# Performance work log

Hardware: AMD Instinct MI355X
Metric: run time of the kernel (lower is better)

The kernel has to match this reference:

```python
import jax, jax.numpy as jnp
import numpy as np

N_NODES = 50000
N_EDGES = 800000
D_IN = 128
D_HID = 128
N_CLASSES = 16
N_GRAPHS = 256


def _gcn_norm(edge_index, num_nodes):
    # PyG GCNConv default: add self-loops, symmetric normalization.
    loops = jnp.arange(num_nodes, dtype=edge_index.dtype)
    src = jnp.concatenate([edge_index[0], loops])
    dst = jnp.concatenate([edge_index[1], loops])
    deg = jax.ops.segment_sum(jnp.ones_like(src, dtype=jnp.float32), dst,
                              num_segments=num_nodes)
    dinv = jnp.where(deg > 0, jax.lax.rsqrt(deg), 0.0)
    norm = dinv[src] * dinv[dst]  # [E + N]
    return src, dst, norm


def _gcn_conv(x, src, dst, norm, W, b, num_nodes):
    h = x @ W                                  # [N, d_out] dense GEMM
    msg = h[src] * norm[:, None]               # gather + scale [E+N, d_out]
    agg = jax.ops.segment_sum(msg, dst, num_segments=num_nodes)
    return agg + b


def setup_inputs() -> dict:
    key = jax.random.key(0)
    ks = jax.random.split(key, 10)
    x = jax.random.normal(ks[0], (N_NODES, D_IN), dtype=jnp.float32)
    edge_index = jax.random.randint(ks[1], (2, N_EDGES), 0, N_NODES, dtype=jnp.int64)
    batch = jnp.sort(jax.random.randint(ks[2], (N_NODES,), 0, N_GRAPHS, dtype=jnp.int64))
    s1 = 1.0 / np.sqrt(D_IN)
    s2 = 1.0 / np.sqrt(D_HID)
    W1 = jax.random.uniform(ks[3], (D_IN, D_HID), jnp.float32, -s1, s1)
    b1 = jnp.zeros((D_HID,), jnp.float32)
    W2 = jax.random.uniform(ks[4], (D_HID, D_HID), jnp.float32, -s2, s2)
    b2 = jnp.zeros((D_HID,), jnp.float32)
    Wc = jax.random.uniform(ks[5], (D_HID, N_CLASSES), jnp.float32, -s2, s2)
    bc = jnp.zeros((N_CLASSES,), jnp.float32)
    return {"x": x, "edge_index": edge_index, "batch": batch,
            "W1": W1, "b1": b1, "W2": W2, "b2": b2, "Wc": Wc, "bc": bc}


def reference(x, edge_index, batch, W1, b1, W2, b2, Wc, bc):
    src, dst, norm = _gcn_norm(edge_index, N_NODES)
    h = _gcn_conv(x, src, dst, norm, W1, b1, N_NODES)
    h = jax.nn.relu(h)  # dropout is identity in eval mode
    h = _gcn_conv(h, src, dst, norm, W2, b2, N_NODES)
    # global mean pool over graph ids
    sums = jax.ops.segment_sum(h, batch, num_segments=N_GRAPHS)
    cnts = jax.ops.segment_sum(jnp.ones((N_NODES,), jnp.float32), batch,
                               num_segments=N_GRAPHS)
    pooled = sums / jnp.maximum(cnts, 1.0)[:, None]  # [G, D_HID]
    return pooled @ Wc + bc  # [G, N_CLASSES]
```

## Files before the change

### kernel.cpp

```cpp
#include <hip/hip_runtime.h>

#define N_NODES 50000
#define N_EDGES 800000
#define D 128
#define N_GRAPHS 256
#define N_CLASSES 16
#define NB_DINV ((N_NODES + 255) / 256)
#define BKT 64

typedef unsigned short ushort_t;
typedef unsigned int uint_t;
typedef unsigned char uchar_t;
typedef __attribute__((ext_vector_type(8))) short bf16x8;
typedef __attribute__((ext_vector_type(4))) float f32x4;
typedef __attribute__((ext_vector_type(4))) int i32x4;

__device__ __forceinline__ float bf2f(uint_t u) {
  return __uint_as_float(u << 16);
}
__device__ __forceinline__ uint_t f2bf(float f) {
  uint_t x = __float_as_uint(f);
  return (x + 0x7fffu + ((x >> 16) & 1u)) >> 16;
}
__device__ __forceinline__ void add8(float* acc, uint4 v) {
  acc[0] += bf2f(v.x & 0xffffu);
  acc[1] += bf2f(v.x >> 16);
  acc[2] += bf2f(v.y & 0xffffu);
  acc[3] += bf2f(v.y >> 16);
  acc[4] += bf2f(v.z & 0xffffu);
  acc[5] += bf2f(v.z >> 16);
  acc[6] += bf2f(v.w & 0xffffu);
  acc[7] += bf2f(v.w >> 16);
}

__global__ void k_pre(const int* __restrict__ ei, int* __restrict__ deg,
                      int* __restrict__ csr) {
  int e = blockIdx.x * blockDim.x + threadIdx.x;
  if (e >= N_EDGES) return;
  int s = ei[e];
  int d = ei[N_EDGES + e];
  int r = atomicAdd(&deg[d], 1);
  if (r < BKT) __builtin_nontemporal_store(s, csr + d * BKT + r);
}

__global__ __launch_bounds__(256) void k_prep(const int* __restrict__ deg,
                                              float* __restrict__ dinv,
                                              const float* __restrict__ W1,
                                              const float* __restrict__ W2,
                                              uint4* __restrict__ W1f,
                                              uint4* __restrict__ W2f,
                                              const int* __restrict__ batch,
                                              float* __restrict__ rcnts) {
  int t = threadIdx.x;
  int b = blockIdx.x;
  if (b < NB_DINV) {
    int i = b * 256 + t;
    if (i < N_NODES) dinv[i] = rsqrtf((float)(deg[i] + 1));
    return;
  }
  if (b < NB_DINV + 16) {
    int slot = (b - NB_DINV) * 256 + t;
    const float* W = (slot < 2048) ? W1 : W2;
    uint4* Wf = (slot < 2048) ? W1f : W2f;
    int sl = slot & 2047;
    int lane = sl & 63;
    int s = (sl >> 6) & 3;
    int n = sl >> 8;
    int col = n * 16 + (lane & 15);
    int k0 = s * 32 + (lane >> 4) * 8;
    uint4 o;
    o.x = f2bf(W[(size_t)(k0 + 0) * D + col]) | (f2bf(W[(size_t)(k0 + 1) * D + col]) << 16);
    o.y = f2bf(W[(size_t)(k0 + 2) * D + col]) | (f2bf(W[(size_t)(k0 + 3) * D + col]) << 16);
    o.z = f2bf(W[(size_t)(k0 + 4) * D + col]) | (f2bf(W[(size_t)(k0 + 5) * D + col]) << 16);
    o.w = f2bf(W[(size_t)(k0 + 6) * D + col]) | (f2bf(W[(size_t)(k0 + 7) * D + col]) << 16);
    Wf[sl] = o;
    return;
  }
  __shared__ int bound[257];
  {
    int g = t;
    int lo = 0, hi = N_NODES;
    while (lo < hi) {
      int m = (lo + hi) >> 1;
      if (batch[m] < g) lo = m + 1; else hi = m;
    }
    bound[g] = lo;
    if (t == 255) bound[256] = N_NODES;
  }
  __syncthreads();
  int cnt = bound[t + 1] - bound[t];
  rcnts[t] = 1.0f / (float)max(cnt, 1);
}

template <typename TIN>
__global__ __launch_bounds__(256) void k_gemm_mfma(const TIN* __restrict__ A,
                                                   const uint4* __restrict__ Wf,
                                                   const float* __restrict__ dinv,
                                                   ushort_t* __restrict__ Out) {
  __shared__ uint4 As[1024];
  int t = threadIdx.x;
  int row0 = blockIdx.x * 64;
  if constexpr (sizeof(TIN) == 4) {
    uint2* As2 = (uint2*)As;
#pragma unroll
    for (int i = 0; i < 8; ++i) {
      int F = t + 256 * i;
      int r = F >> 5, f = F & 31;
      int grow = row0 + r;
      uint2 u = make_uint2(0, 0);
      if (grow < N_NODES) {
        float4 v = *(const float4*)(A + (size_t)grow * D + f * 4);
        u.x = f2bf(v.x) | (f2bf(v.y) << 16);
        u.y = f2bf(v.z) | (f2bf(v.w) << 16);
      }
      int g = f >> 1;
      As2[(r * 16 + (g ^ (r & 7))) * 2 + (f & 1)] = u;
    }
  } else {
#pragma unroll
    for (int i = 0; i < 4; ++i) {
      int G = t + 256 * i;
      int r = G >> 4, g = G & 15;
      int grow = row0 + r;
      uint4 u = make_uint4(0, 0, 0, 0);
      if (grow < N_NODES) u = *(const uint4*)(A + (size_t)grow * D + g * 8);
      As[r * 16 + (g ^ (r & 7))] = u;
    }
  }
  __syncthreads();
  int wv = t >> 6, lane = t & 63;
  int row16 = lane & 15, chunk = lane >> 4;
  int rl = wv * 16 + row16;
  bf16x8 afrag[4];
#pragma unroll
  for (int s = 0; s < 4; ++s) {
    int g = s * 4 + chunk;
    afrag[s] = *(const bf16x8*)&As[rl * 16 + (g ^ (rl & 7))];
  }
  f32x4 acc[8];
#pragma unroll
  for (int n = 0; n < 8; ++n) acc[n] = (f32x4){0.f, 0.f, 0.f, 0.f};
  const bf16x8* Wb = (const bf16x8*)Wf;
#pragma unroll
  for (int n = 0; n < 8; ++n) {
#pragma unroll
    for (int s = 0; s < 4; ++s) {
      bf16x8 b = Wb[(n * 4 + s) * 64 + lane];
      acc[n] = __builtin_amdgcn_mfma_f32_16x16x32_bf16(afrag[s], b, acc[n], 0, 0, 0);
    }
  }
  int row0w = row0 + wv * 16;
  int crow0 = row0w + chunk * 4;
  float dv[4];
#pragma unroll
  for (int j = 0; j < 4; ++j)
    dv[j] = (crow0 + j < N_NODES) ? dinv[crow0 + j] : 0.f;
#pragma unroll
  for (int n = 0; n < 8; ++n) {
#pragma unroll
    for (int j = 0; j < 4; ++j) {
      int r = crow0 + j;
      if (r < N_NODES)
        Out[(size_t)r * D + n * 16 + row16] = (ushort_t)f2bf(acc[n][j] * dv[j]);
    }
  }
}

__device__ __forceinline__ void agg_core(const ushort_t* __restrict__ h,
                                         const int* __restrict__ csr,
                                         int beg, int end, int grp, int d0,
                                         float* acc) {
  for (int wb = beg; wb < end; wb += 16) {
    int i0 = wb + grp * 4;
    i32x4 s4 = __builtin_nontemporal_load((const i32x4*)(csr + i0));
    bool b0 = i0 < end, b1 = i0 + 1 < end, b2 = i0 + 2 < end, b3 = i0 + 3 < end;
    uint4 v0, v1, v2, v3;
    if (b0) v0 = *(const uint4*)(h + (size_t)s4.x * D + d0);
    if (b1) v1 = *(const uint4*)(h + (size_t)s4.y * D + d0);
    if (b2) v2 = *(const uint4*)(h + (size_t)s4.z * D + d0);
    if (b3) v3 = *(const uint4*)(h + (size_t)s4.w * D + d0);
    if (b0) add8(acc, v0);
    if (b1) add8(acc, v1);
    if (b2) add8(acc, v2);
    if (b3) add8(acc, v3);
  }
}

__global__ __launch_bounds__(256) void k_agg_relu(const ushort_t* __restrict__ h,
                                                  const int* __restrict__ csr,
                                                  const int* __restrict__ deg,
                                                  const float* __restrict__ dinv,
                                                  const float* __restrict__ bias,
                                                  ushort_t* __restrict__ obf) {
  int t = threadIdx.x;
  int wv = t >> 6, lane = t & 63;
  int grp = lane >> 4, gl = lane & 15;
  int d0 = gl * 8;
  int node = blockIdx.x * 4 + wv;
  int beg = node * BKT, end = beg + min(deg[node], BKT);
  float acc[8] = {0.f, 0.f, 0.f, 0.f, 0.f, 0.f, 0.f, 0.f};
  agg_core(h, csr, beg, end, grp, d0, acc);
#pragma unroll
  for (int m = 16; m <= 32; m <<= 1) {
#pragma unroll
    for (int i = 0; i < 8; ++i) acc[i] += __shfl_xor(acc[i], m);
  }
  if (grp == 0) {
    uint4 v = *(const uint4*)(h + (size_t)node * D + d0);
    add8(acc, v);
    float sc = dinv[node];
    float4 blo = *(const float4*)(bias + d0);
    float4 bhi = *(const float4*)(bias + d0 + 4);
    acc[0] = fmaf(acc[0], sc, blo.x);
    acc[1] = fmaf(acc[1], sc, blo.y);
    acc[2] = fmaf(acc[2], sc, blo.z);
    acc[3] = fmaf(acc[3], sc, blo.w);
    acc[4] = fmaf(acc[4], sc, bhi.x);
    acc[5] = fmaf(acc[5], sc, bhi.y);
    acc[6] = fmaf(acc[6], sc, bhi.z);
    acc[7] = fmaf(acc[7], sc, bhi.w);
#pragma unroll
    for (int i = 0; i < 8; ++i) acc[i] = fmaxf(acc[i], 0.f);
    uint4 o;
    o.x = f2bf(acc[0]) | (f2bf(acc[1]) << 16);
    o.y = f2bf(acc[2]) | (f2bf(acc[3]) << 16);
    o.z = f2bf(acc[4]) | (f2bf(acc[5]) << 16);
    o.w = f2bf(acc[6]) | (f2bf(acc[7]) << 16);
    *(uint4*)(obf + (size_t)node * D + d0) = o;
  }
}

__global__ __launch_bounds__(1024) void k_agg_pool(const ushort_t* __restrict__ h,
                                                   const int* __restrict__ csr,
                                                   const int* __restrict__ deg,
                                                   const float* __restrict__ dinv,
                                                   const int* __restrict__ batch,
                                                   const float* __restrict__ rcnts,
                                                   float* __restrict__ sums) {
  __shared__ float pool2[16][128];
  int t = threadIdx.x;
  int wv = t >> 6, lane = t & 63;
  int grp = lane >> 4, gl = lane & 15;
  int d0 = gl * 8;
  int node0 = blockIdx.x * 16;
  int node = node0 + wv;
  int g0 = batch[node0];
  int beg = node * BKT, end = beg + min(deg[node], BKT);
  float acc[8] = {0.f, 0.f, 0.f, 0.f, 0.f, 0.f, 0.f, 0.f};
  agg_core(h, csr, beg, end, grp, d0, acc);
#pragma unroll
  for (int m = 16; m <= 32; m <<= 1) {
#pragma unroll
    for (int k = 0; k < 8; ++k) acc[k] += __shfl_xor(acc[k], m);
  }
  if (grp == 0) {
    uint4 v = *(const uint4*)(h + (size_t)node * D + d0);
    add8(acc, v);
    int g = batch[node];
    float sc = dinv[node] * rcnts[g];
    if (g == g0) {
#pragma unroll
      for (int k = 0; k < 8; ++k) pool2[wv][d0 + k] = acc[k] * sc;
    } else {
#pragma unroll
      for (int k = 0; k < 8; ++k) {
        pool2[wv][d0 + k] = 0.f;
        atomicAdd(&sums[(size_t)g * D + d0 + k], acc[k] * sc);
      }
    }
  }
  __syncthreads();
  if (t < 128) {
    float s = 0.f;
#pragma unroll
    for (int w = 0; w < 16; ++w) s += pool2[w][t];
    atomicAdd(&sums[(size_t)g0 * D + t], s);
  }
}

__global__ __launch_bounds__(128) void k_final(const float* __restrict__ sums,
                                               const float* __restrict__ b2,
                                               const float* __restrict__ Wc,
                                               const float* __restrict__ bc,
                                               float* __restrict__ out) {
  __shared__ float p[128];
  int g = blockIdx.x;
  int t = threadIdx.x;
  p[t] = sums[g * D + t] + b2[t];
  __syncthreads();
  if (t < N_CLASSES) {
    float acc = bc[t];
    for (int k = 0; k < D; ++k) acc = fmaf(p[k], Wc[k * N_CLASSES + t], acc);
    out[g * N_CLASSES + t] = acc;
  }
}

extern "C" void kernel_launch(void* const* d_in, const int* in_sizes, int n_in,
                              void* d_out, int out_size, void* d_ws, size_t ws_size,
                              hipStream_t stream) {
  const float* x = (const float*)d_in[0];
  const int* ei = (const int*)d_in[1];
  const int* batch = (const int*)d_in[2];
  const float* W1 = (const float*)d_in[3];
  const float* b1 = (const float*)d_in[4];
  const float* W2 = (const float*)d_in[5];
  const float* b2 = (const float*)d_in[6];
  const float* Wc = (const float*)d_in[7];
  const float* bc = (const float*)d_in[8];
  float* out = (float*)d_out;

  char* ws = (char*)d_ws;
  size_t off = 0;
  auto alloc = [&](size_t bytes) -> void* {
    void* p = (void*)(ws + off);
    off += (bytes + 255) & ~(size_t)255;
    return p;
  };
  int* deg = (int*)alloc((size_t)N_NODES * 4);
  float* sums = (float*)alloc((size_t)N_GRAPHS * D * 4);
  size_t zero_bytes = off;
  float* dinv = (float*)alloc((size_t)N_NODES * 4);
  float* rcnts = (float*)alloc((size_t)N_GRAPHS * 4);
  uint4* W1f = (uint4*)alloc((size_t)2048 * 16);
  uint4* W2f = (uint4*)alloc((size_t)2048 * 16);
  int* csr = (int*)alloc((size_t)N_NODES * BKT * 4);
  ushort_t* hbuf = (ushort_t*)alloc((size_t)N_NODES * D * 2);
  ushort_t* x2 = (ushort_t*)alloc((size_t)N_NODES * D * 2);

  hipMemsetAsync(ws, 0, zero_bytes, stream);

  k_pre<<<(N_EDGES + 255) / 256, 256, 0, stream>>>(ei, deg, csr);
  k_prep<<<NB_DINV + 17, 256, 0, stream>>>(deg, dinv, W1, W2, W1f, W2f, batch, rcnts);

  k_gemm_mfma<float><<<(N_NODES + 63) / 64, 256, 0, stream>>>(x, W1f, dinv, hbuf);
  k_agg_relu<<<N_NODES / 4, 256, 0, stream>>>(hbuf, csr, deg, dinv, b1, x2);
  k_gemm_mfma<ushort_t><<<(N_NODES + 63) / 64, 256, 0, stream>>>(x2, W2f, dinv, hbuf);
  k_agg_pool<<<N_NODES / 16, 1024, 0, stream>>>(hbuf, csr, deg, dinv, batch, rcnts, sums);

  k_final<<<N_GRAPHS, 128, 0, stream>>>(sums, b2, Wc, bc, out);
}
```

Measured before the change: 249.4 us.

## Merge CSR build with first GEMM and apply source degree norm during aggregation

Removes the separate dinv array and the dinv scaling in the GEMM epilogue. Aggregation now computes rsqrt(deg+1) per gathered source edge and uses an FMA in place of the add. Because the GEMM no longer needs dinv, the edge-bucketing work and the first GEMM run as disjoint block ranges of one kernel, saving a launch and letting the two overlap. The cost is an extra scattered deg load and rsqrt per edge in both aggregation kernels, plus mixing atomic-heavy blocks with GEMM blocks in one grid.

```diff
diff --git a/kernel.cpp b/kernel.cpp
--- a/kernel.cpp
+++ b/kernel.cpp
@@ -5,12 +5,12 @@
 #define D 128
 #define N_GRAPHS 256
 #define N_CLASSES 16
-#define NB_DINV ((N_NODES + 255) / 256)
 #define BKT 64
+#define NGEMM ((N_NODES + 63) / 64)
+#define NPRE ((N_EDGES + 255) / 256)
 
 typedef unsigned short ushort_t;
 typedef unsigned int uint_t;
-typedef unsigned char uchar_t;
 typedef __attribute__((ext_vector_type(8))) short bf16x8;
 typedef __attribute__((ext_vector_type(4))) float f32x4;
 typedef __attribute__((ext_vector_type(4))) int i32x4;
@@ -22,44 +22,27 @@
   uint_t x = __float_as_uint(f);
   return (x + 0x7fffu + ((x >> 16) & 1u)) >> 16;
 }
-__device__ __forceinline__ void add8(float* acc, uint4 v) {
-  acc[0] += bf2f(v.x & 0xffffu);
-  acc[1] += bf2f(v.x >> 16);
-  acc[2] += bf2f(v.y & 0xffffu);
-  acc[3] += bf2f(v.y >> 16);
-  acc[4] += bf2f(v.z & 0xffffu);
-  acc[5] += bf2f(v.z >> 16);
-  acc[6] += bf2f(v.w & 0xffffu);
-  acc[7] += bf2f(v.w >> 16);
-}
-
-__global__ void k_pre(const int* __restrict__ ei, int* __restrict__ deg,
-                      int* __restrict__ csr) {
-  int e = blockIdx.x * blockDim.x + threadIdx.x;
-  if (e >= N_EDGES) return;
-  int s = ei[e];
-  int d = ei[N_EDGES + e];
-  int r = atomicAdd(&deg[d], 1);
-  if (r < BKT) __builtin_nontemporal_store(s, csr + d * BKT + r);
-}
-
-__global__ __launch_bounds__(256) void k_prep(const int* __restrict__ deg,
-                                              float* __restrict__ dinv,
-                                              const float* __restrict__ W1,
-                                              const float* __restrict__ W2,
-                                              uint4* __restrict__ W1f,
-                                              uint4* __restrict__ W2f,
-                                              const int* __restrict__ batch,
-                                              float* __restrict__ rcnts) {
+__device__ __forceinline__ void fma8(float* acc, float w, uint4 v) {
+  acc[0] = fmaf(w, bf2f(v.x & 0xffffu), acc[0]);
+  acc[1] = fmaf(w, bf2f(v.x >> 16), acc[1]);
+  acc[2] = fmaf(w, bf2f(v.y & 0xffffu), acc[2]);
+  acc[3] = fmaf(w, bf2f(v.y >> 16), acc[3]);
+  acc[4] = fmaf(w, bf2f(v.z & 0xffffu), acc[4]);
+  acc[5] = fmaf(w, bf2f(v.z >> 16), acc[5]);
+  acc[6] = fmaf(w, bf2f(v.w & 0xffffu), acc[6]);
+  acc[7] = fmaf(w, bf2f(v.w >> 16), acc[7]);
+}
+
+__global__ __launch_bounds__(256) void k_prep0(const float* __restrict__ W1,
+                                               const float* __restrict__ W2,
+                                               uint4* __restrict__ W1f,
+                                               uint4* __restrict__ W2f,
+                                               const int* __restrict__ batch,
+                                               float* __restrict__ rcnts) {
   int t = threadIdx.x;
   int b = blockIdx.x;
-  if (b < NB_DINV) {
-    int i = b * 256 + t;
-    if (i < N_NODES) dinv[i] = rsqrtf((float)(deg[i] + 1));
-    return;
-  }
-  if (b < NB_DINV + 16) {
-    int slot = (b - NB_DINV) * 256 + t;
+  if (b < 16) {
+    int slot = b * 256 + t;
     const float* W = (slot < 2048) ? W1 : W2;
     uint4* Wf = (slot < 2048) ? W1f : W2f;
     int sl = slot & 2047;
@@ -93,13 +76,11 @@
 }
 
 template <typename TIN>
-__global__ __launch_bounds__(256) void k_gemm_mfma(const TIN* __restrict__ A,
-                                                   const uint4* __restrict__ Wf,
-                                                   const float* __restrict__ dinv,
-                                                   ushort_t* __restrict__ Out) {
-  __shared__ uint4 As[1024];
-  int t = threadIdx.x;
-  int row0 = blockIdx.x * 64;
+__device__ __forceinline__ void gemm_body(const TIN* __restrict__ A,
+                                          const uint4* __restrict__ Wf,
+                                          ushort_t* __restrict__ Out,
+                                          uint4* As, int bid, int t) {
+  int row0 = bid * 64;
   if constexpr (sizeof(TIN) == 4) {
     uint2* As2 = (uint2*)As;
 #pragma unroll
@@ -149,25 +130,50 @@
       acc[n] = __builtin_amdgcn_mfma_f32_16x16x32_bf16(afrag[s], b, acc[n], 0, 0, 0);
     }
   }
-  int row0w = row0 + wv * 16;
-  int crow0 = row0w + chunk * 4;
-  float dv[4];
-#pragma unroll
-  for (int j = 0; j < 4; ++j)
-    dv[j] = (crow0 + j < N_NODES) ? dinv[crow0 + j] : 0.f;
+  int crow0 = row0 + wv * 16 + chunk * 4;
 #pragma unroll
   for (int n = 0; n < 8; ++n) {
 #pragma unroll
     for (int j = 0; j < 4; ++j) {
       int r = crow0 + j;
       if (r < N_NODES)
-        Out[(size_t)r * D + n * 16 + row16] = (ushort_t)f2bf(acc[n][j] * dv[j]);
-    }
-  }
+        Out[(size_t)r * D + n * 16 + row16] = (ushort_t)f2bf(acc[n][j]);
+    }
+  }
+}
+
+__global__ __launch_bounds__(256) void k_mega(const float* __restrict__ x,
+                                              const int* __restrict__ ei,
+                                              const uint4* __restrict__ W1f,
+                                              int* __restrict__ deg,
+                                              int* __restrict__ csr,
+                                              ushort_t* __restrict__ hbuf) {
+  __shared__ uint4 As[1024];
+  int t = threadIdx.x;
+  int b = blockIdx.x;
+  if (b < NPRE) {
+    int e = b * 256 + t;
+    if (e < N_EDGES) {
+      int s = ei[e];
+      int d = ei[N_EDGES + e];
+      int r = atomicAdd(&deg[d], 1);
+      if (r < BKT) __builtin_nontemporal_store(s, csr + d * BKT + r);
+    }
+    return;
+  }
+  gemm_body<float>(x, W1f, hbuf, As, b - NPRE, t);
+}
+
+__global__ __launch_bounds__(256) void k_gemm2(const ushort_t* __restrict__ A,
+                                               const uint4* __restrict__ Wf,
+                                               ushort_t* __restrict__ Out) {
+  __shared__ uint4 As[1024];
+  gemm_body<ushort_t>(A, Wf, Out, As, blockIdx.x, threadIdx.x);
 }
 
 __device__ __forceinline__ void agg_core(const ushort_t* __restrict__ h,
                                          const int* __restrict__ csr,
+                                         const int* __restrict__ deg,
                                          int beg, int end, int grp, int d0,
                                          float* acc) {
   for (int wb = beg; wb < end; wb += 16) {
@@ -175,21 +181,21 @@
     i32x4 s4 = __builtin_nontemporal_load((const i32x4*)(csr + i0));
     bool b0 = i0 < end, b1 = i0 + 1 < end, b2 = i0 + 2 < end, b3 = i0 + 3 < end;
     uint4 v0, v1, v2, v3;
-    if (b0) v0 = *(const uint4*)(h + (size_t)s4.x * D + d0);
-    if (b1) v1 = *(const uint4*)(h + (size_t)s4.y * D + d0);
-    if (b2) v2 = *(const uint4*)(h + (size_t)s4.z * D + d0);
-    if (b3) v3 = *(const uint4*)(h + (size_t)s4.w * D + d0);
-    if (b0) add8(acc, v0);
-    if (b1) add8(acc, v1);
-    if (b2) add8(acc, v2);
-    if (b3) add8(acc, v3);
+    float w0 = 0.f, w1 = 0.f, w2 = 0.f, w3 = 0.f;
+    if (b0) { v0 = *(const uint4*)(h + (size_t)s4.x * D + d0); w0 = rsqrtf((float)(deg[s4.x] + 1)); }
+    if (b1) { v1 = *(const uint4*)(h + (size_t)s4.y * D + d0); w1 = rsqrtf((float)(deg[s4.y] + 1)); }
+    if (b2) { v2 = *(const uint4*)(h + (size_t)s4.z * D + d0); w2 = rsqrtf((float)(deg[s4.z] + 1)); }
+    if (b3) { v3 = *(const uint4*)(h + (size_t)s4.w * D + d0); w3 = rsqrtf((float)(deg[s4.w] + 1)); }
+    if (b0) fma8(acc, w0, v0);
+    if (b1) fma8(acc, w1, v1);
+    if (b2) fma8(acc, w2, v2);
+    if (b3) fma8(acc, w3, v3);
   }
 }
 
 __global__ __launch_bounds__(256) void k_agg_relu(const ushort_t* __restrict__ h,
                                                   const int* __restrict__ csr,
                                                   const int* __restrict__ deg,
-                                                  const float* __restrict__ dinv,
                                                   const float* __restrict__ bias,
                                                   ushort_t* __restrict__ obf) {
   int t = threadIdx.x;
@@ -197,28 +203,29 @@
   int grp = lane >> 4, gl = lane & 15;
   int d0 = gl * 8;
   int node = blockIdx.x * 4 + wv;
-  int beg = node * BKT, end = beg + min(deg[node], BKT);
+  int dn_i = deg[node];
+  int beg = node * BKT, end = beg + min(dn_i, BKT);
   float acc[8] = {0.f, 0.f, 0.f, 0.f, 0.f, 0.f, 0.f, 0.f};
-  agg_core(h, csr, beg, end, grp, d0, acc);
+  agg_core(h, csr, deg, beg, end, grp, d0, acc);
 #pragma unroll
   for (int m = 16; m <= 32; m <<= 1) {
 #pragma unroll
     for (int i = 0; i < 8; ++i) acc[i] += __shfl_xor(acc[i], m);
   }
   if (grp == 0) {
+    float dn = rsqrtf((float)(dn_i + 1));
     uint4 v = *(const uint4*)(h + (size_t)node * D + d0);
-    add8(acc, v);
-    float sc = dinv[node];
+    fma8(acc, dn, v);
     float4 blo = *(const float4*)(bias + d0);
     float4 bhi = *(const float4*)(bias + d0 + 4);
-    acc[0] = fmaf(acc[0], sc, blo.x);
-    acc[1] = fmaf(acc[1], sc, blo.y);
-    acc[2] = fmaf(acc[2], sc, blo.z);
-    acc[3] = fmaf(acc[3], sc, blo.w);
-    acc[4] = fmaf(acc[4], sc, bhi.x);
-    acc[5] = fmaf(acc[5], sc, bhi.y);
-    acc[6] = fmaf(acc[6], sc, bhi.z);
-    acc[7] = fmaf(acc[7], sc, bhi.w);
+    acc[0] = fmaf(acc[0], dn, blo.x);
+    acc[1] = fmaf(acc[1], dn, blo.y);
+    acc[2] = fmaf(acc[2], dn, blo.z);
+    acc[3] = fmaf(acc[3], dn, blo.w);
+    acc[4] = fmaf(acc[4], dn, bhi.x);
+    acc[5] = fmaf(acc[5], dn, bhi.y);
+    acc[6] = fmaf(acc[6], dn, bhi.z);
+    acc[7] = fmaf(acc[7], dn, bhi.w);
 #pragma unroll
     for (int i = 0; i < 8; ++i) acc[i] = fmaxf(acc[i], 0.f);
     uint4 o;
@@ -233,7 +240,6 @@
 __global__ __launch_bounds__(1024) void k_agg_pool(const ushort_t* __restrict__ h,
                                                    const int* __restrict__ csr,
                                                    const int* __restrict__ deg,
-                                                   const float* __restrict__ dinv,
                                                    const int* __restrict__ batch,
                                                    const float* __restrict__ rcnts,
                                                    float* __restrict__ sums) {
@@ -245,19 +251,21 @@
   int node0 = blockIdx.x * 16;
   int node = node0 + wv;
   int g0 = batch[node0];
-  int beg = node * BKT, end = beg + min(deg[node], BKT);
+  int dn_i = deg[node];
+  int beg = node * BKT, end = beg + min(dn_i, BKT);
   float acc[8] = {0.f, 0.f, 0.f, 0.f, 0.f, 0.f, 0.f, 0.f};
-  agg_core(h, csr, beg, end, grp, d0, acc);
+  agg_core(h, csr, deg, beg, end, grp, d0, acc);
 #pragma unroll
   for (int m = 16; m <= 32; m <<= 1) {
 #pragma unroll
     for (int k = 0; k < 8; ++k) acc[k] += __shfl_xor(acc[k], m);
   }
   if (grp == 0) {
+    float dn = rsqrtf((float)(dn_i + 1));
     uint4 v = *(const uint4*)(h + (size_t)node * D + d0);
-    add8(acc, v);
+    fma8(acc, dn, v);
     int g = batch[node];
-    float sc = dinv[node] * rcnts[g];
+    float sc = dn * rcnts[g];
     if (g == g0) {
 #pragma unroll
       for (int k = 0; k < 8; ++k) pool2[wv][d0 + k] = acc[k] * sc;
@@ -319,7 +327,6 @@
   int* deg = (int*)alloc((size_t)N_NODES * 4);
   float* sums = (float*)alloc((size_t)N_GRAPHS * D * 4);
   size_t zero_bytes = off;
-  float* dinv = (float*)alloc((size_t)N_NODES * 4);
   float* rcnts = (float*)alloc((size_t)N_GRAPHS * 4);
   uint4* W1f = (uint4*)alloc((size_t)2048 * 16);
   uint4* W2f = (uint4*)alloc((size_t)2048 * 16);
@@ -329,13 +336,10 @@
 
   hipMemsetAsync(ws, 0, zero_bytes, stream);
 
-  k_pre<<<(N_EDGES + 255) / 256, 256, 0, stream>>>(ei, deg, csr);
-  k_prep<<<NB_DINV + 17, 256, 0, stream>>>(deg, dinv, W1, W2, W1f, W2f, batch, rcnts);
-
-  k_gemm_mfma<float><<<(N_NODES + 63) / 64, 256, 0, stream>>>(x, W1f, dinv, hbuf);
-  k_agg_relu<<<N_NODES / 4, 256, 0, stream>>>(hbuf, csr, deg, dinv, b1, x2);
-  k_gemm_mfma<ushort_t><<<(N_NODES + 63) / 64, 256, 0, stream>>>(x2, W2f, dinv, hbuf);
-  k_agg_pool<<<N_NODES / 16, 1024, 0, stream>>>(hbuf, csr, deg, dinv, batch, rcnts, sums);
-
+  k_prep0<<<17, 256, 0, stream>>>(W1, W2, W1f, W2f, batch, rcnts);
+  k_mega<<<NPRE + NGEMM, 256, 0, stream>>>(x, ei, (const uint4*)W1f, deg, csr, hbuf);
+  k_agg_relu<<<N_NODES / 4, 256, 0, stream>>>(hbuf, csr, deg, b1, x2);
+  k_gemm2<<<NGEMM, 256, 0, stream>>>(x2, (const uint4*)W2f, hbuf);
+  k_agg_pool<<<N_NODES / 16, 1024, 0, stream>>>(hbuf, csr, deg, batch, rcnts, sums);
   k_final<<<N_GRAPHS, 128, 0, stream>>>(sums, b2, Wc, bc, out);
 }
```

After: 266.1 us. 1.07x slower.
